# Kernel tuning notes

Measured on AMD Instinct MI355X. Metric: run time of the kernel, lower is better.

Reference implementation:

```python
import jax, jax.numpy as jnp
import numpy as np

# Constants from UpFIRDn2dJIT(channel=64, lrelu_upsampling=2, filter_size=6, kernel_size=3)
# with init_kernel(in_size=128, out_size=128): up_factor = dn_factor = 2.
UP = 2
DN = 2
SLOPE = 0.2
GAIN = 1.4142135623730951  # sqrt(2)
CROP = 1  # kernel_size - 1 - kernel_size//2 for kernel_size=3
IN_SIZE = 128
FILTER_SIZE = 6
B, C = 8, 64


def _firwin_lowpass(numtaps, cutoff, width, fs):
    # Reproduces scipy.signal.firwin(numtaps, cutoff, width=width, fs=fs)
    # (lowpass, pass_zero=True, scale=True, Kaiser window from `width`).
    nyq = 0.5 * fs
    atten = 2.285 * (numtaps - 1) * np.pi * (width / nyq) + 7.95  # kaiser_atten
    if atten > 50:
        beta = 0.1102 * (atten - 8.7)
    elif atten > 21:
        beta = 0.5842 * (atten - 21) ** 0.4 + 0.07886 * (atten - 21)
    else:
        beta = 0.0
    m = np.arange(numtaps) - (numtaps - 1) / 2.0
    c = cutoff / nyq
    h = c * np.sinc(c * m) * np.kaiser(numtaps, beta)
    h = h / h.sum()  # scale so DC gain == 1
    return h.astype(np.float32)


def _conv1d_same(x, f, axis):
    # x: [N, 1, H, W]; 1D cross-correlation along `axis` (2 or 3) with torch
    # padding='same' semantics for even taps: left pad = (K-1)//2, right pad gets the extra.
    K = f.shape[0]
    pl = (K - 1) // 2
    pr = (K - 1) - pl
    if axis == 2:
        kern = f.reshape(1, 1, K, 1)
        pad = [(pl, pr), (0, 0)]
    else:
        kern = f.reshape(1, 1, 1, K)
        pad = [(0, 0), (pl, pr)]
    return jax.lax.conv_general_dilated(
        x, kern, window_strides=(1, 1), padding=pad,
        dimension_numbers=("NCHW", "OIHW", "NCHW"))


def _forward(x, bias, up_filter, dn_filter):
    x = x[:, :, CROP:-CROP, CROP:-CROP]            # [B, C, 128, 128]
    b, c, h, w = x.shape
    x = x + bias[None, :, None, None]
    x = x.reshape(b * c, 1, h, w)
    x = jnp.repeat(jnp.repeat(x, UP, axis=2), UP, axis=3)
    # outer(f, f) conv == separable 1D convs (filter is an outer product)
    x = _conv1d_same(_conv1d_same(x, up_filter, 2), up_filter, 3)
    x = jnp.where(x >= 0, x, SLOPE * x) * GAIN     # leaky ReLU * gain
    x = _conv1d_same(_conv1d_same(x, dn_filter, 2), dn_filter, 3)
    x = x[:, :, ::DN, ::DN]                        # grid_pool2d -> [B*C, 1, 128, 128]
    return x.reshape(b, c, x.shape[2], x.shape[3])


def setup_inputs() -> dict:
    key = jax.random.key(0)
    kx, = jax.random.split(key, 1)
    x = jax.random.normal(kx, (B, C, IN_SIZE + 2 * CROP, IN_SIZE + 2 * CROP), dtype=jnp.float32)
    bias = jnp.zeros((C,), dtype=jnp.float32)  # nn.Parameter init to zeros
    taps = FILTER_SIZE * UP  # 12
    up_filter = jnp.asarray(_firwin_lowpass(taps, IN_SIZE / 2.0001, IN_SIZE, IN_SIZE))
    dn_filter = jnp.asarray(_firwin_lowpass(taps, IN_SIZE / 2.0001, IN_SIZE, IN_SIZE))
    return {"x": x, "bias": bias, "up_filter": up_filter, "dn_filter": dn_filter}


def reference(x, bias, up_filter, dn_filter):
    return _forward(x, bias, up_filter, dn_filter)
```

## Files before the change

kernel.cpp:

```cpp
#include <hip/hip_runtime.h>


#define GAIN_C 1.4142135623730951f
#define NEG_C ((0.2f - 1.0f) * GAIN_C)

typedef short v8s __attribute__((ext_vector_type(8)));
typedef float v4f __attribute__((ext_vector_type(4)));

__device__ __forceinline__ int f2bf(float f) {
    unsigned u = __float_as_uint(f);
    return (int)((u + 0x7FFFu + ((u >> 16) & 1u)) >> 16) & 0xFFFF;
}
__device__ __forceinline__ int pack_bf2(float a, float b) {
#if __has_builtin(__builtin_amdgcn_cvt_pk_bf16_f32)
    typedef __bf16 bf2 __attribute__((ext_vector_type(2)));
    bf2 r = __builtin_amdgcn_cvt_pk_bf16_f32(a, b);
    int o; __builtin_memcpy(&o, &r, 4); return o;
#else
    return f2bf(a) | (f2bf(b) << 16);
#endif
}

__device__ float band(int x, int q, int qlim, int xlim, const float* fu) {
    if (q >= qlim || x >= xlim || x < 0) return 0.f;
    int p = q >> 1, d = x - p;
    if (q & 1) {
        if (d < 0 || d > 6) return 0.f;
        if (d == 0) return fu[0];
        if (d == 6) return fu[11];
        return fu[2 * d - 1] + fu[2 * d];
    } else {
        if (d < 0 || d > 5) return 0.f;
        return fu[2 * d] + fu[2 * d + 1];
    }
}
__device__ float dband(int o, int q, int v, int qlim, const float* fd) {
    if (q >= qlim || q < 0) return 0.f;
    if (v == 0 && q < 5) return 0.f;
    if (v == 2 && q >= qlim - 5) return 0.f;
    int k = q - 2 * o;
    if (k < 0 || k > 11) return 0.f;
    return fd[k];
}

__global__ __launch_bounds__(256) void build_consts(
    const float* __restrict__ fu, const float* __restrict__ fd,
    short* __restrict__ ws)
{
    int idx = blockIdx.x * 256 + threadIdx.x;
    int l = (idx >> 3) & 63, j = idx & 7;
    int l15 = l & 15, kq = (l >> 4) * 8 + j;
    float val;
    if (idx < 2560) {
        int nt = idx >> 9;
        int k0 = 8 * nt < 16 ? 8 * nt : 16;
        val = band(k0 + kq, 16 * nt + l15, 74, 43, fu);
    } else if (idx < 7168) {
        int mt = (idx - 2560) >> 9;
        int k0 = 8 * mt < 48 ? 8 * mt : 48;
        val = band(k0 + kq, 16 * mt + l15, 138, 75, fu);
    } else if (idx < 15360) {
        int rel = idx - 7168;
        int v = (rel >> 12) ? 2 : 0;
        int fi = (rel & 4095) >> 9;
        int mt = fi >> 1, kt = fi & 1;
        int k0 = 32 * mt < 80 ? 32 * mt : 80;
        val = dband(16 * mt + l15, k0 + 32 * kt + kq, v, 138, fd);
    } else {
        int rel = idx - 15360;
        int v = rel >> 11, fi = (rel & 2047) >> 9;
        int nt = fi >> 1, kt = fi & 1;
        int k0 = nt ? 16 : 0;
        val = dband(16 * nt + l15, k0 + 32 * kt + kq, v, 74, fd);
    }
    ws[idx] = (short)f2bf(val);
}

#define XPITCH 48
#define BPITCH 88
#define UPITCH 152
#define TPITCH 88

__global__ __launch_bounds__(512, 8) void upfirdn_mfma(
    const float* __restrict__ xin_all,
    const float* __restrict__ bias,
    const short* __restrict__ cws,
    float* __restrict__ out)
{
    __shared__ __align__(16) short SH[19200];
    short* B1t = SH;
    short* Ut  = SH + 7040;
    short* Xl  = SH + 7040;
    short* T   = SH;

    const int tid  = threadIdx.x;
    const int lane = tid & 63, w = tid >> 6;
    const int l15  = lane & 15, q4 = lane >> 4;
    const int bx = blockIdx.x, by = blockIdx.y, bc = blockIdx.z;
    const int i0 = by * 64, j0 = bx * 32;

    const short* GtB = cws;
    const short* G2A = cws + 2560;
    const short* DA  = cws + 7168  + (by ? 4096 : 0);
    const short* D2B = cws + 15360 + ((bx == 0) ? 0 : (bx == 3) ? 2 : 1) * 2048;

    {
        const float* xp = xin_all + (size_t)bc * (130 * 130);
        const float bv = bias[bc & 63];
        const bool colInt = (bx == 1) | (bx == 2);
        int* Xli = (int*)Xl;
        for (int idx = tid; idx < 1920; idx += 512) {
            int r = idx / 24, cp = idx - r * 24;
            int gr = i0 - 5 + r;
            float f0 = 0.f, f1 = 0.f;
            if (r < 75 && (unsigned)gr < 128u && cp < 22) {
                const float* rowp = xp + (gr + 1) * 130 + 1;
                int gc0 = j0 - 5 + 2 * cp;
                if (colInt) {
                    f0 = rowp[gc0] + bv;
                    if (cp < 21) f1 = rowp[gc0 + 1] + bv;
                } else {
                    if ((unsigned)gc0 < 128u) f0 = rowp[gc0] + bv;
                    if (cp < 21 && (unsigned)(gc0 + 1) < 128u)
                        f1 = rowp[gc0 + 1] + bv;
                }
            }
            Xli[r * 24 + cp] = pack_bf2(f0, f1);
        }
    }
    __syncthreads();

    for (int t = w; t < 25; t += 8) {
        const int mt = t / 5, nt = t - mt * 5;
        const int k0 = 8 * nt < 16 ? 8 * nt : 16;
        v8s bf = *(const v8s*)&GtB[nt * 512 + lane * 8];
        v8s a  = *(const v8s*)&Xl[(16 * mt + l15) * XPITCH + k0 + q4 * 8];
        v4f acc = {0.f, 0.f, 0.f, 0.f};
        acc = __builtin_amdgcn_mfma_f32_16x16x32_bf16(a, bf, acc, 0, 0, 0);
        *(int2*)&B1t[(16 * nt + l15) * BPITCH + 16 * mt + q4 * 4] =
            make_int2(pack_bf2(acc[0], acc[1]), pack_bf2(acc[2], acc[3]));
    }
    __syncthreads();

    for (int t = w; t < 45; t += 8) {
        const int mt = t / 5, nt = t - mt * 5;
        const int k0 = 8 * mt < 48 ? 8 * mt : 48;
        v8s af = *(const v8s*)&G2A[mt * 512 + lane * 8];
        v8s b  = *(const v8s*)&B1t[(16 * nt + l15) * BPITCH + k0 + q4 * 8];
        v4f acc = {0.f, 0.f, 0.f, 0.f};
        acc = __builtin_amdgcn_mfma_f32_16x16x32_bf16(af, b, acc, 0, 0, 0);
#pragma unroll
        for (int i = 0; i < 4; ++i)
            acc[i] = GAIN_C * acc[i] + NEG_C * fminf(acc[i], 0.f);
        *(int2*)&Ut[(16 * nt + l15) * UPITCH + 16 * mt + q4 * 4] =
            make_int2(pack_bf2(acc[0], acc[1]), pack_bf2(acc[2], acc[3]));
    }
    __syncthreads();

    for (int t = w; t < 20; t += 8) {
        const int mt = t / 5, nt = t - mt * 5;
        const int k0 = 32 * mt < 80 ? 32 * mt : 80;
        v4f acc = {0.f, 0.f, 0.f, 0.f};
#pragma unroll
        for (int kt = 0; kt < 2; ++kt) {
            v8s a = *(const v8s*)&DA[(mt * 2 + kt) * 512 + lane * 8];
            v8s b = *(const v8s*)&Ut[(16 * nt + l15) * UPITCH
                                     + k0 + 32 * kt + q4 * 8];
            acc = __builtin_amdgcn_mfma_f32_16x16x32_bf16(a, b, acc, 0, 0, 0);
        }
#pragma unroll
        for (int i = 0; i < 4; ++i)
            T[(16 * mt + q4 * 4 + i) * TPITCH + 16 * nt + l15] =
                (short)f2bf(acc[i]);
    }
    __syncthreads();

    {
        const int mt = w >> 1, nt = w & 1;
        const int k0 = nt ? 16 : 0;
        v4f acc = {0.f, 0.f, 0.f, 0.f};
#pragma unroll
        for (int kt = 0; kt < 2; ++kt) {
            v8s a = *(const v8s*)&T[(16 * mt + l15) * TPITCH + k0 + 32 * kt + q4 * 8];
            v8s b = *(const v8s*)&D2B[(nt * 2 + kt) * 512 + lane * 8];
            acc = __builtin_amdgcn_mfma_f32_16x16x32_bf16(a, b, acc, 0, 0, 0);
        }
        float* op = out + (size_t)bc * 16384
                  + (size_t)(i0 + 16 * mt + q4 * 4) * 128 + (j0 + 16 * nt + l15);
#pragma unroll
        for (int i = 0; i < 4; ++i) op[i * 128] = acc[i];
    }
}

extern "C" void kernel_launch(void* const* d_in, const int* in_sizes, int n_in,
                              void* d_out, int out_size, void* d_ws, size_t ws_size,
                              hipStream_t stream) {
    const float* x  = (const float*)d_in[0];
    const float* bs = (const float*)d_in[1];
    const float* fu = (const float*)d_in[2];
    const float* fd = (const float*)d_in[3];
    float* outp = (float*)d_out;
    short* ws = (short*)d_ws;

    build_consts<<<84, 256, 0, stream>>>(fu, fd, ws);
    upfirdn_mfma<<<dim3(4, 2, 512), 512, 0, stream>>>(x, bs, ws, outp);
}
```

Before: 120.6 us.

## Fuse per-wave column-strip stages via register bpermute, drop two barriers

Each block now runs 5 waves instead of 8, and each wave owns one 16-column strip through the first three MFMA stages. Stage-1 output goes to a private LDS slice. The stage-2 upsampled tile stays in registers and is reshuffled with ds_bpermute to form stage-3 operands, which removes the Ut LDS buffer and two block barriers. The input load is also vectorised to 8 elements per thread. The trade-off is more register pressure and fewer waves per block, with some waves idle in the final stage.

```diff
diff --git a/kernel.cpp b/kernel.cpp
--- a/kernel.cpp
+++ b/kernel.cpp
@@ -78,20 +78,17 @@
 
 #define XPITCH 48
 #define BPITCH 88
-#define UPITCH 152
-#define TPITCH 88
-
-__global__ __launch_bounds__(512, 8) void upfirdn_mfma(
+#define TPITCH 80
+
+__global__ __launch_bounds__(320, 6) void upfirdn_mfma(
     const float* __restrict__ xin_all,
     const float* __restrict__ bias,
     const short* __restrict__ cws,
     float* __restrict__ out)
 {
-    __shared__ __align__(16) short SH[19200];
-    short* B1t = SH;
-    short* Ut  = SH + 7040;
-    short* Xl  = SH + 7040;
-    short* T   = SH;
+    __shared__ __align__(16) short SH[16000];
+    short* Xl = SH;
+    short* T  = SH + 10880;
 
     const int tid  = threadIdx.x;
     const int lane = tid & 63, w = tid >> 6;
@@ -99,6 +96,8 @@
     const int bx = blockIdx.x, by = blockIdx.y, bc = blockIdx.z;
     const int i0 = by * 64, j0 = bx * 32;
 
+    short* Bsl = SH + 3840 + w * 1408;
+
     const short* GtB = cws;
     const short* G2A = cws + 2560;
     const short* DA  = cws + 7168  + (by ? 4096 : 0);
@@ -108,85 +107,124 @@
         const float* xp = xin_all + (size_t)bc * (130 * 130);
         const float bv = bias[bc & 63];
         const bool colInt = (bx == 1) | (bx == 2);
-        int* Xli = (int*)Xl;
-        for (int idx = tid; idx < 1920; idx += 512) {
-            int r = idx / 24, cp = idx - r * 24;
-            int gr = i0 - 5 + r;
-            float f0 = 0.f, f1 = 0.f;
-            if (r < 75 && (unsigned)gr < 128u && cp < 22) {
-                const float* rowp = xp + (gr + 1) * 130 + 1;
-                int gc0 = j0 - 5 + 2 * cp;
-                if (colInt) {
-                    f0 = rowp[gc0] + bv;
-                    if (cp < 21) f1 = rowp[gc0 + 1] + bv;
-                } else {
-                    if ((unsigned)gc0 < 128u) f0 = rowp[gc0] + bv;
-                    if (cp < 21 && (unsigned)(gc0 + 1) < 128u)
-                        f1 = rowp[gc0 + 1] + bv;
+        for (int s = tid; s < 480; s += 320) {
+            const int r  = s / 6, c6 = s - 6 * r;
+            const int gr = i0 - 5 + r;
+            int* dst = (int*)Xl + r * 24 + 4 * c6;
+            if (r < 75 && (unsigned)gr < 128u) {
+                const float* rowp = xp + (gr + 1) * 130 + 1 + (j0 - 5);
+                float f[8];
+#pragma unroll
+                for (int j = 0; j < 8; ++j) {
+                    const int c = 8 * c6 + j;
+                    bool v = c < 43;
+                    if (!colInt) v = v && ((unsigned)(j0 - 5 + c) < 128u);
+                    f[j] = v ? rowp[c] + bv : 0.f;
                 }
+                *(int2*)dst = make_int2(pack_bf2(f[0], f[1]), pack_bf2(f[2], f[3]));
+                *(int2*)(dst + 2) =
+                    make_int2(pack_bf2(f[4], f[5]), pack_bf2(f[6], f[7]));
+            } else {
+                *(int2*)dst = make_int2(0, 0);
+                *(int2*)(dst + 2) = make_int2(0, 0);
             }
-            Xli[r * 24 + cp] = pack_bf2(f0, f1);
         }
     }
     __syncthreads();
 
-    for (int t = w; t < 25; t += 8) {
-        const int mt = t / 5, nt = t - mt * 5;
-        const int k0 = 8 * nt < 16 ? 8 * nt : 16;
-        v8s bf = *(const v8s*)&GtB[nt * 512 + lane * 8];
-        v8s a  = *(const v8s*)&Xl[(16 * mt + l15) * XPITCH + k0 + q4 * 8];
+
+    {
+        const int k0c = 8 * w < 16 ? 8 * w : 16;
+        v8s bf = *(const v8s*)&GtB[w * 512 + lane * 8];
+#pragma unroll
+        for (int mt = 0; mt < 5; ++mt) {
+            v8s a = *(const v8s*)&Xl[(16 * mt + l15) * XPITCH + k0c + q4 * 8];
+            v4f acc = {0.f, 0.f, 0.f, 0.f};
+            acc = __builtin_amdgcn_mfma_f32_16x16x32_bf16(a, bf, acc, 0, 0, 0);
+            *(int2*)&Bsl[l15 * BPITCH + 16 * mt + 4 * q4] =
+                make_int2(pack_bf2(acc[0], acc[1]), pack_bf2(acc[2], acc[3]));
+        }
+    }
+
+    int uw[9][2];
+    {
+#pragma unroll
+        for (int mt = 0; mt < 9; ++mt) {
+            const int k0 = 8 * mt < 48 ? 8 * mt : 48;
+            v8s af = *(const v8s*)&G2A[mt * 512 + lane * 8];
+            v8s b  = *(const v8s*)&Bsl[l15 * BPITCH + k0 + q4 * 8];
+            v4f acc = {0.f, 0.f, 0.f, 0.f};
+            acc = __builtin_amdgcn_mfma_f32_16x16x32_bf16(af, b, acc, 0, 0, 0);
+#pragma unroll
+            for (int j = 0; j < 4; ++j)
+                acc[j] = GAIN_C * acc[j] + NEG_C * fminf(acc[j], 0.f);
+            uw[mt][0] = pack_bf2(acc[0], acc[1]);
+            uw[mt][1] = pack_bf2(acc[2], acc[3]);
+        }
+    }
+
+    {
+        const int idx0 = (l15 + 16 * ((2 * q4) & 3)) * 4;
+        const int idx1 = (l15 + 16 * ((2 * q4 + 1) & 3)) * 4;
+        const bool hi = (lane >= 32);
+
+#define BUILDF(S16, DST)                                                     \
+    {                                                                        \
+        int a0 = __builtin_amdgcn_ds_bpermute(idx0, uw[S16][0]);             \
+        int b0 = __builtin_amdgcn_ds_bpermute(idx0, uw[(S16) + 1][0]);       \
+        int a1 = __builtin_amdgcn_ds_bpermute(idx0, uw[S16][1]);             \
+        int b1 = __builtin_amdgcn_ds_bpermute(idx0, uw[(S16) + 1][1]);       \
+        int a2 = __builtin_amdgcn_ds_bpermute(idx1, uw[S16][0]);             \
+        int b2 = __builtin_amdgcn_ds_bpermute(idx1, uw[(S16) + 1][0]);       \
+        int a3 = __builtin_amdgcn_ds_bpermute(idx1, uw[S16][1]);             \
+        int b3 = __builtin_amdgcn_ds_bpermute(idx1, uw[(S16) + 1][1]);       \
+        union { int i[4]; v8s v; } u_;                                       \
+        u_.i[0] = hi ? b0 : a0; u_.i[1] = hi ? b1 : a1;                      \
+        u_.i[2] = hi ? b2 : a2; u_.i[3] = hi ? b3 : a3;                      \
+        DST = u_.v;                                                          \
+    }
+
+        v8s F0, F2, F4, F5, F6, F7;
+        BUILDF(0, F0); BUILDF(2, F2); BUILDF(4, F4);
+        BUILDF(5, F5); BUILDF(6, F6); BUILDF(7, F7);
+#undef BUILDF
+
+#define S3TILE(AMT, FA, FB)                                                  \
+    {                                                                        \
+        v8s a0 = *(const v8s*)&DA[((AMT) * 2 + 0) * 512 + lane * 8];         \
+        v8s a1 = *(const v8s*)&DA[((AMT) * 2 + 1) * 512 + lane * 8];         \
+        v4f acc = {0.f, 0.f, 0.f, 0.f};                                      \
+        acc = __builtin_amdgcn_mfma_f32_16x16x32_bf16(a0, FA, acc, 0, 0, 0); \
+        acc = __builtin_amdgcn_mfma_f32_16x16x32_bf16(a1, FB, acc, 0, 0, 0); \
+        int p01 = pack_bf2(acc[0], acc[1]);                                  \
+        int p23 = pack_bf2(acc[2], acc[3]);                                  \
+        short* tb = &T[(16 * (AMT) + 4 * q4) * TPITCH + 16 * w + l15];       \
+        tb[0 * TPITCH] = (short)p01; tb[1 * TPITCH] = (short)(p01 >> 16);    \
+        tb[2 * TPITCH] = (short)p23; tb[3 * TPITCH] = (short)(p23 >> 16);    \
+    }
+        S3TILE(0, F0, F2)
+        S3TILE(1, F2, F4)
+        S3TILE(2, F4, F6)
+        S3TILE(3, F5, F7)
+#undef S3TILE
+    }
+    __syncthreads();
+
+#pragma unroll
+    for (int rep = 0; rep < 2; ++rep) {
+        const int q = w + rep * 5;
+        if (rep == 1 && w >= 3) break;
+        const int mt = q >> 1, nt = q & 1;
+        const int k0 = nt ? 16 : 0;
+        v8s a0 = *(const v8s*)&T[(16 * mt + l15) * TPITCH + k0 + q4 * 8];
+        v8s a1 = *(const v8s*)&T[(16 * mt + l15) * TPITCH + k0 + 32 + q4 * 8];
+        v8s b0 = *(const v8s*)&D2B[(nt * 2 + 0) * 512 + lane * 8];
+        v8s b1 = *(const v8s*)&D2B[(nt * 2 + 1) * 512 + lane * 8];
         v4f acc = {0.f, 0.f, 0.f, 0.f};
-        acc = __builtin_amdgcn_mfma_f32_16x16x32_bf16(a, bf, acc, 0, 0, 0);
-        *(int2*)&B1t[(16 * nt + l15) * BPITCH + 16 * mt + q4 * 4] =
-            make_int2(pack_bf2(acc[0], acc[1]), pack_bf2(acc[2], acc[3]));
-    }
-    __syncthreads();
-
-    for (int t = w; t < 45; t += 8) {
-        const int mt = t / 5, nt = t - mt * 5;
-        const int k0 = 8 * mt < 48 ? 8 * mt : 48;
-        v8s af = *(const v8s*)&G2A[mt * 512 + lane * 8];
-        v8s b  = *(const v8s*)&B1t[(16 * nt + l15) * BPITCH + k0 + q4 * 8];
-        v4f acc = {0.f, 0.f, 0.f, 0.f};
-        acc = __builtin_amdgcn_mfma_f32_16x16x32_bf16(af, b, acc, 0, 0, 0);
-#pragma unroll
-        for (int i = 0; i < 4; ++i)
-            acc[i] = GAIN_C * acc[i] + NEG_C * fminf(acc[i], 0.f);
-        *(int2*)&Ut[(16 * nt + l15) * UPITCH + 16 * mt + q4 * 4] =
-            make_int2(pack_bf2(acc[0], acc[1]), pack_bf2(acc[2], acc[3]));
-    }
-    __syncthreads();
-
-    for (int t = w; t < 20; t += 8) {
-        const int mt = t / 5, nt = t - mt * 5;
-        const int k0 = 32 * mt < 80 ? 32 * mt : 80;
-        v4f acc = {0.f, 0.f, 0.f, 0.f};
-#pragma unroll
-        for (int kt = 0; kt < 2; ++kt) {
-            v8s a = *(const v8s*)&DA[(mt * 2 + kt) * 512 + lane * 8];
-            v8s b = *(const v8s*)&Ut[(16 * nt + l15) * UPITCH
-                                     + k0 + 32 * kt + q4 * 8];
-            acc = __builtin_amdgcn_mfma_f32_16x16x32_bf16(a, b, acc, 0, 0, 0);
-        }
-#pragma unroll
-        for (int i = 0; i < 4; ++i)
-            T[(16 * mt + q4 * 4 + i) * TPITCH + 16 * nt + l15] =
-                (short)f2bf(acc[i]);
-    }
-    __syncthreads();
-
-    {
-        const int mt = w >> 1, nt = w & 1;
-        const int k0 = nt ? 16 : 0;
-        v4f acc = {0.f, 0.f, 0.f, 0.f};
-#pragma unroll
-        for (int kt = 0; kt < 2; ++kt) {
-            v8s a = *(const v8s*)&T[(16 * mt + l15) * TPITCH + k0 + 32 * kt + q4 * 8];
-            v8s b = *(const v8s*)&D2B[(nt * 2 + kt) * 512 + lane * 8];
-            acc = __builtin_amdgcn_mfma_f32_16x16x32_bf16(a, b, acc, 0, 0, 0);
-        }
+        acc = __builtin_amdgcn_mfma_f32_16x16x32_bf16(a0, b0, acc, 0, 0, 0);
+        acc = __builtin_amdgcn_mfma_f32_16x16x32_bf16(a1, b1, acc, 0, 0, 0);
         float* op = out + (size_t)bc * 16384
-                  + (size_t)(i0 + 16 * mt + q4 * 4) * 128 + (j0 + 16 * nt + l15);
+                  + (size_t)(i0 + 16 * mt + 4 * q4) * 128 + (j0 + 16 * nt + l15);
 #pragma unroll
         for (int i = 0; i < 4; ++i) op[i * 128] = acc[i];
     }
@@ -203,5 +241,5 @@
     short* ws = (short*)d_ws;
 
     build_consts<<<84, 256, 0, stream>>>(fu, fd, ws);
-    upfirdn_mfma<<<dim3(4, 2, 512), 512, 0, stream>>>(x, bs, ws, outp);
-}
+    upfirdn_mfma<<<dim3(4, 2, 512), 320, 0, stream>>>(x, bs, ws, outp);
+}
```

Measured after the change: 124.9 us. +3.6%, slower.

## Process two channels per block to reuse filter constants and balance MFMA work

Applied to the files above, without the earlier changes.

Each block now handles two channel planes (bc and bc+256), so every filter-matrix fragment loaded from global memory feeds two MFMAs, and the grid is halved. Work tiles are split across the 8 waves in static, balanced, unrolled chunks instead of strided loops. Input loading is restructured so each thread reads 8 contiguous columns for both channels. The cost is double the shared memory (76.8 KB dynamic), lower occupancy (launch bounds 4), and more register pressure.

```diff
diff --git a/kernel.cpp b/kernel.cpp
--- a/kernel.cpp
+++ b/kernel.cpp
@@ -80,18 +80,121 @@
 #define BPITCH 88
 #define UPITCH 152
 #define TPITCH 88
-
-__global__ __launch_bounds__(512, 8) void upfirdn_mfma(
+#define CHSTRIDE 19200
+
+template<int K>
+__device__ __forceinline__ void s1_chunk(
+    int base, const short* __restrict__ GtB,
+    const short* __restrict__ Xl0, const short* __restrict__ Xl1,
+    short* __restrict__ B1t0, short* __restrict__ B1t1,
+    int lane, int l15, int q4)
+{
+#pragma unroll
+    for (int i = 0; i < K; ++i) {
+        const int t = base + i;
+        const int mt = t / 5, nt = t - mt * 5;
+        const int k0 = 8 * nt < 16 ? 8 * nt : 16;
+        v8s bf = *(const v8s*)&GtB[nt * 512 + lane * 8];
+        const int aoff = (16 * mt + l15) * XPITCH + k0 + q4 * 8;
+        v8s aA = *(const v8s*)&Xl0[aoff];
+        v8s aB = *(const v8s*)&Xl1[aoff];
+        v4f z = {0.f, 0.f, 0.f, 0.f};
+        v4f accA = __builtin_amdgcn_mfma_f32_16x16x32_bf16(aA, bf, z, 0, 0, 0);
+        v4f accB = __builtin_amdgcn_mfma_f32_16x16x32_bf16(aB, bf, z, 0, 0, 0);
+        const int dst = (16 * nt + l15) * BPITCH + 16 * mt + q4 * 4;
+        *(int2*)&B1t0[dst] = make_int2(pack_bf2(accA[0], accA[1]),
+                                       pack_bf2(accA[2], accA[3]));
+        *(int2*)&B1t1[dst] = make_int2(pack_bf2(accB[0], accB[1]),
+                                       pack_bf2(accB[2], accB[3]));
+    }
+}
+
+template<int K>
+__device__ __forceinline__ void s2_chunk(
+    int base, const short* __restrict__ G2A,
+    const short* __restrict__ B1t0, const short* __restrict__ B1t1,
+    short* __restrict__ Ut0, short* __restrict__ Ut1,
+    int lane, int l15, int q4)
+{
+#pragma unroll
+    for (int i = 0; i < K; ++i) {
+        const int t = base + i;
+        const int mt = t / 5, nt = t - mt * 5;
+        const int k0 = 8 * mt < 48 ? 8 * mt : 48;
+        v8s af = *(const v8s*)&G2A[mt * 512 + lane * 8];
+        const int boff = (16 * nt + l15) * BPITCH + k0 + q4 * 8;
+        v8s bA = *(const v8s*)&B1t0[boff];
+        v8s bB = *(const v8s*)&B1t1[boff];
+        v4f z = {0.f, 0.f, 0.f, 0.f};
+        v4f accA = __builtin_amdgcn_mfma_f32_16x16x32_bf16(af, bA, z, 0, 0, 0);
+        v4f accB = __builtin_amdgcn_mfma_f32_16x16x32_bf16(af, bB, z, 0, 0, 0);
+#pragma unroll
+        for (int j = 0; j < 4; ++j) {
+            accA[j] = GAIN_C * accA[j] + NEG_C * fminf(accA[j], 0.f);
+            accB[j] = GAIN_C * accB[j] + NEG_C * fminf(accB[j], 0.f);
+        }
+        const int dst = (16 * nt + l15) * UPITCH + 16 * mt + q4 * 4;
+        *(int2*)&Ut0[dst] = make_int2(pack_bf2(accA[0], accA[1]),
+                                      pack_bf2(accA[2], accA[3]));
+        *(int2*)&Ut1[dst] = make_int2(pack_bf2(accB[0], accB[1]),
+                                      pack_bf2(accB[2], accB[3]));
+    }
+}
+
+template<int K>
+__device__ __forceinline__ void s3_chunk(
+    int base, const short* __restrict__ DA,
+    const short* __restrict__ Ut0, const short* __restrict__ Ut1,
+    short* __restrict__ T0, short* __restrict__ T1,
+    int lane, int l15, int q4)
+{
+#pragma unroll
+    for (int i = 0; i < K; ++i) {
+        const int t = base + i;
+        const int mt = t / 5, nt = t - mt * 5;
+        const int k0 = 32 * mt < 80 ? 32 * mt : 80;
+        v8s a0 = *(const v8s*)&DA[(mt * 2 + 0) * 512 + lane * 8];
+        v8s a1 = *(const v8s*)&DA[(mt * 2 + 1) * 512 + lane * 8];
+        const int boff = (16 * nt + l15) * UPITCH + k0 + q4 * 8;
+        v8s b0A = *(const v8s*)&Ut0[boff];
+        v8s b1A = *(const v8s*)&Ut0[boff + 32];
+        v8s b0B = *(const v8s*)&Ut1[boff];
+        v8s b1B = *(const v8s*)&Ut1[boff + 32];
+        v4f accA = {0.f, 0.f, 0.f, 0.f};
+        v4f accB = {0.f, 0.f, 0.f, 0.f};
+        accA = __builtin_amdgcn_mfma_f32_16x16x32_bf16(a0, b0A, accA, 0, 0, 0);
+        accB = __builtin_amdgcn_mfma_f32_16x16x32_bf16(a0, b0B, accB, 0, 0, 0);
+        accA = __builtin_amdgcn_mfma_f32_16x16x32_bf16(a1, b1A, accA, 0, 0, 0);
+        accB = __builtin_amdgcn_mfma_f32_16x16x32_bf16(a1, b1B, accB, 0, 0, 0);
+        const int toff = (16 * mt + q4 * 4) * TPITCH + 16 * nt + l15;
+        int pA01 = pack_bf2(accA[0], accA[1]);
+        int pA23 = pack_bf2(accA[2], accA[3]);
+        int pB01 = pack_bf2(accB[0], accB[1]);
+        int pB23 = pack_bf2(accB[2], accB[3]);
+        short* tA = (short*)&T0[toff];
+        short* tB = (short*)&T1[toff];
+        tA[0 * TPITCH] = (short)pA01; tA[1 * TPITCH] = (short)(pA01 >> 16);
+        tA[2 * TPITCH] = (short)pA23; tA[3 * TPITCH] = (short)(pA23 >> 16);
+        tB[0 * TPITCH] = (short)pB01; tB[1 * TPITCH] = (short)(pB01 >> 16);
+        tB[2 * TPITCH] = (short)pB23; tB[3 * TPITCH] = (short)(pB23 >> 16);
+    }
+}
+
+__global__ __launch_bounds__(512, 4) void upfirdn_mfma(
     const float* __restrict__ xin_all,
     const float* __restrict__ bias,
     const short* __restrict__ cws,
     float* __restrict__ out)
 {
-    __shared__ __align__(16) short SH[19200];
-    short* B1t = SH;
-    short* Ut  = SH + 7040;
-    short* Xl  = SH + 7040;
-    short* T   = SH;
+    extern __shared__ short SH[];
+    short* B1t0 = SH;
+    short* Ut0  = SH + 7040;
+    short* Xl0  = SH + 7040;
+    short* T0   = SH;
+    short* B1t1 = SH + CHSTRIDE;
+    short* Ut1  = SH + CHSTRIDE + 7040;
+    short* Xl1  = SH + CHSTRIDE + 7040;
+    short* T1   = SH + CHSTRIDE;
 
     const int tid  = threadIdx.x;
     const int lane = tid & 63, w = tid >> 6;
@@ -104,91 +207,78 @@
     const short* DA  = cws + 7168  + (by ? 4096 : 0);
     const short* D2B = cws + 15360 + ((bx == 0) ? 0 : (bx == 3) ? 2 : 1) * 2048;
 
-    {
-        const float* xp = xin_all + (size_t)bc * (130 * 130);
-        const float bv = bias[bc & 63];
-        const bool colInt = (bx == 1) | (bx == 2);
-        int* Xli = (int*)Xl;
-        for (int idx = tid; idx < 1920; idx += 512) {
-            int r = idx / 24, cp = idx - r * 24;
-            int gr = i0 - 5 + r;
-            float f0 = 0.f, f1 = 0.f;
-            if (r < 75 && (unsigned)gr < 128u && cp < 22) {
-                const float* rowp = xp + (gr + 1) * 130 + 1;
-                int gc0 = j0 - 5 + 2 * cp;
-                if (colInt) {
-                    f0 = rowp[gc0] + bv;
-                    if (cp < 21) f1 = rowp[gc0 + 1] + bv;
-                } else {
-                    if ((unsigned)gc0 < 128u) f0 = rowp[gc0] + bv;
-                    if (cp < 21 && (unsigned)(gc0 + 1) < 128u)
-                        f1 = rowp[gc0 + 1] + bv;
-                }
+    if (tid < 480) {
+        const int r  = tid / 6, c6 = tid - 6 * r;
+        const int gr = i0 - 5 + r;
+        int* dst0 = (int*)Xl0 + r * 24 + 4 * c6;
+        int* dst1 = (int*)Xl1 + r * 24 + 4 * c6;
+        if (r < 75 && (unsigned)gr < 128u) {
+            const float* rowp0 = xin_all + (size_t)bc * (130 * 130)
+                               + (gr + 1) * 130 + 1 + (j0 - 5);
+            const float* rowp1 = rowp0 + (size_t)256 * (130 * 130);
+            const float bv = bias[bc & 63];
+            const bool colInt = (bx == 1) | (bx == 2);
+            float fA[8], fB[8];
+#pragma unroll
+            for (int j = 0; j < 8; ++j) {
+                const int c = 8 * c6 + j;
+                bool v = c < 43;
+                if (!colInt) v = v && ((unsigned)(j0 - 5 + c) < 128u);
+                fA[j] = v ? rowp0[c] + bv : 0.f;
+                fB[j] = v ? rowp1[c] + bv : 0.f;
             }
-            Xli[r * 24 + cp] = pack_bf2(f0, f1);
+            *(int2*)dst0 = make_int2(pack_bf2(fA[0], fA[1]), pack_bf2(fA[2], fA[3]));
+            *(int2*)(dst0 + 2) =
+                make_int2(pack_bf2(fA[4], fA[5]), pack_bf2(fA[6], fA[7]));
+            *(int2*)dst1 = make_int2(pack_bf2(fB[0], fB[1]), pack_bf2(fB[2], fB[3]));
+            *(int2*)(dst1 + 2) =
+                make_int2(pack_bf2(fB[4], fB[5]), pack_bf2(fB[6], fB[7]));
+        } else {
+            *(int2*)dst0 = make_int2(0, 0);
+            *(int2*)(dst0 + 2) = make_int2(0, 0);
+            *(int2*)dst1 = make_int2(0, 0);
+            *(int2*)(dst1 + 2) = make_int2(0, 0);
         }
     }
     __syncthreads();
 
-    for (int t = w; t < 25; t += 8) {
-        const int mt = t / 5, nt = t - mt * 5;
-        const int k0 = 8 * nt < 16 ? 8 * nt : 16;
-        v8s bf = *(const v8s*)&GtB[nt * 512 + lane * 8];
-        v8s a  = *(const v8s*)&Xl[(16 * mt + l15) * XPITCH + k0 + q4 * 8];
-        v4f acc = {0.f, 0.f, 0.f, 0.f};
-        acc = __builtin_amdgcn_mfma_f32_16x16x32_bf16(a, bf, acc, 0, 0, 0);
-        *(int2*)&B1t[(16 * nt + l15) * BPITCH + 16 * mt + q4 * 4] =
-            make_int2(pack_bf2(acc[0], acc[1]), pack_bf2(acc[2], acc[3]));
-    }
-    __syncthreads();
-
-    for (int t = w; t < 45; t += 8) {
-        const int mt = t / 5, nt = t - mt * 5;
-        const int k0 = 8 * mt < 48 ? 8 * mt : 48;
-        v8s af = *(const v8s*)&G2A[mt * 512 + lane * 8];
-        v8s b  = *(const v8s*)&B1t[(16 * nt + l15) * BPITCH + k0 + q4 * 8];
-        v4f acc = {0.f, 0.f, 0.f, 0.f};
-        acc = __builtin_amdgcn_mfma_f32_16x16x32_bf16(af, b, acc, 0, 0, 0);
-#pragma unroll
-        for (int i = 0; i < 4; ++i)
-            acc[i] = GAIN_C * acc[i] + NEG_C * fminf(acc[i], 0.f);
-        *(int2*)&Ut[(16 * nt + l15) * UPITCH + 16 * mt + q4 * 4] =
-            make_int2(pack_bf2(acc[0], acc[1]), pack_bf2(acc[2], acc[3]));
-    }
-    __syncthreads();
-
-    for (int t = w; t < 20; t += 8) {
-        const int mt = t / 5, nt = t - mt * 5;
-        const int k0 = 32 * mt < 80 ? 32 * mt : 80;
-        v4f acc = {0.f, 0.f, 0.f, 0.f};
-#pragma unroll
-        for (int kt = 0; kt < 2; ++kt) {
-            v8s a = *(const v8s*)&DA[(mt * 2 + kt) * 512 + lane * 8];
-            v8s b = *(const v8s*)&Ut[(16 * nt + l15) * UPITCH
-                                     + k0 + 32 * kt + q4 * 8];
-            acc = __builtin_amdgcn_mfma_f32_16x16x32_bf16(a, b, acc, 0, 0, 0);
-        }
-#pragma unroll
-        for (int i = 0; i < 4; ++i)
-            T[(16 * mt + q4 * 4 + i) * TPITCH + 16 * nt + l15] =
-                (short)f2bf(acc[i]);
-    }
+    if (w == 0) s1_chunk<4>(0,         GtB, Xl0, Xl1, B1t0, B1t1, lane, l15, q4);
+    else        s1_chunk<3>(3 * w + 1, GtB, Xl0, Xl1, B1t0, B1t1, lane, l15, q4);
+    __syncthreads();
+
+    if (w < 5) s2_chunk<6>(6 * w,     G2A, B1t0, B1t1, Ut0, Ut1, lane, l15, q4);
+    else       s2_chunk<5>(5 * w + 5, G2A, B1t0, B1t1, Ut0, Ut1, lane, l15, q4);
+    __syncthreads();
+
+    if (w < 4) s3_chunk<3>(3 * w,     DA, Ut0, Ut1, T0, T1, lane, l15, q4);
+    else       s3_chunk<2>(2 * w + 4, DA, Ut0, Ut1, T0, T1, lane, l15, q4);
     __syncthreads();
 
     {
         const int mt = w >> 1, nt = w & 1;
         const int k0 = nt ? 16 : 0;
-        v4f acc = {0.f, 0.f, 0.f, 0.f};
-#pragma unroll
-        for (int kt = 0; kt < 2; ++kt) {
-            v8s a = *(const v8s*)&T[(16 * mt + l15) * TPITCH + k0 + 32 * kt + q4 * 8];
-            v8s b = *(const v8s*)&D2B[(nt * 2 + kt) * 512 + lane * 8];
-            acc = __builtin_amdgcn_mfma_f32_16x16x32_bf16(a, b, acc, 0, 0, 0);
+        const int aoff = (16 * mt + l15) * TPITCH + k0 + q4 * 8;
+        v8s aA0 = *(const v8s*)&T0[aoff];
+        v8s aA1 = *(const v8s*)&T0[aoff + 32];
+        v8s aB0 = *(const v8s*)&T1[aoff];
+        v8s aB1 = *(const v8s*)&T1[aoff + 32];
+        v8s b0 = *(const v8s*)&D2B[(nt * 2 + 0) * 512 + lane * 8];
+        v8s b1 = *(const v8s*)&D2B[(nt * 2 + 1) * 512 + lane * 8];
+        v4f accA = {0.f, 0.f, 0.f, 0.f};
+        v4f accB = {0.f, 0.f, 0.f, 0.f};
+        accA = __builtin_amdgcn_mfma_f32_16x16x32_bf16(aA0, b0, accA, 0, 0, 0);
+        accB = __builtin_amdgcn_mfma_f32_16x16x32_bf16(aB0, b0, accB, 0, 0, 0);
+        accA = __builtin_amdgcn_mfma_f32_16x16x32_bf16(aA1, b1, accA, 0, 0, 0);
+        accB = __builtin_amdgcn_mfma_f32_16x16x32_bf16(aB1, b1, accB, 0, 0, 0);
+        const size_t obase = (size_t)(i0 + 16 * mt + q4 * 4) * 128
+                           + (j0 + 16 * nt + l15);
+        float* opA = out + (size_t)bc * 16384 + obase;
+        float* opB = opA + (size_t)256 * 16384;
+#pragma unroll
+        for (int i = 0; i < 4; ++i) {
+            opA[i * 128] = accA[i];
+            opB[i * 128] = accB[i];
         }
-        float* op = out + (size_t)bc * 16384
-                  + (size_t)(i0 + 16 * mt + q4 * 4) * 128 + (j0 + 16 * nt + l15);
-#pragma unroll
-        for (int i = 0; i < 4; ++i) op[i * 128] = acc[i];
     }
 }
 
@@ -203,5 +293,5 @@
     short* ws = (short*)d_ws;
 
     build_consts<<<84, 256, 0, stream>>>(fu, fd, ws);
-    upfirdn_mfma<<<dim3(4, 2, 512), 512, 0, stream>>>(x, bs, ws, outp);
-}
+    upfirdn_mfma<<<dim3(4, 2, 256), 512, 76800, stream>>>(x, bs, ws, outp);
+}
```

Result: slower. 126.1 us (+4.6%).
